# Kernel optimization log

Measured on AMD Instinct MI355X. Metric: run time of the kernel, lower is better.

The kernel has to match this reference:

```python
import jax, jax.numpy as jnp
import numpy as np

B, S, D, H = 2, 2048, 1024, 16
HW = D // H  # head width = 64


def setup_inputs() -> dict:
    key = jax.random.key(0)
    ks = jax.random.split(key, 9)
    x = jax.random.normal(ks[0], (B, S, D), dtype=jnp.float32)
    mask = jax.random.randint(ks[1], (B, S), 0, 2, dtype=jnp.int32)
    pos = jax.random.normal(ks[2], (B, S, S), dtype=jnp.float32) * 0.02
    wq = jax.random.normal(ks[3], (D, D), dtype=jnp.float32) * 0.02
    bq = jnp.zeros((D,), dtype=jnp.float32)
    wk = jax.random.normal(ks[4], (D, D), dtype=jnp.float32) * 0.02
    bk = jnp.zeros((D,), dtype=jnp.float32)
    wv = jax.random.normal(ks[5], (D, D), dtype=jnp.float32) * 0.02
    bv = jnp.zeros((D,), dtype=jnp.float32)
    return {"x": x, "mask": mask, "pos": pos,
            "wq": wq, "bq": bq, "wk": wk, "bk": bk, "wv": wv, "bv": bv}


def reference(x, mask, pos, wq, bq, wk, bk, wv, bv):
    # QKV projections (torch Linear: y = x @ W^T + b)
    q = (x @ wq.T + bq).reshape(B, S, H, HW)
    k = (x @ wk.T + bk).reshape(B, S, H, HW)
    v = (x @ wv.T + bv).reshape(B, S, H, HW)
    # scores: (B, H, Sq, Sk)
    scores = jnp.einsum('bqhd,bkhd->bhqk', q, k) / jnp.sqrt(jnp.float32(HW))
    scores = scores + pos[:, None, :, :]
    m = mask.astype(jnp.float32)[:, None, None, :]
    scores = scores - 10000.0 * (1.0 - m)
    attn = jax.nn.softmax(scores, axis=-1)  # dropout p=0 (inference)
    h = jnp.einsum('bhqk,bkhd->bqhd', attn, v).reshape(B, S, D)
    return h
```

## Files before the change

### kernel.cpp

```cpp
#include <hip/hip_runtime.h>

#define B_ 2
#define S_ 2048
#define D_ 1024
#define H_ 16
#define HW_ 64
#define NT_ (S_ / 64)

typedef __attribute__((ext_vector_type(8))) short s16x8;
typedef __attribute__((ext_vector_type(4))) float f32x4;
typedef __attribute__((ext_vector_type(2))) unsigned int u32x2;
typedef __attribute__((ext_vector_type(4))) unsigned int u32x4;

__device__ __forceinline__ unsigned short f2bf(float f) {
  unsigned int x = __builtin_bit_cast(unsigned int, f);
  x += 0x7fffu + ((x >> 16) & 1u);
  return (unsigned short)(x >> 16);
}
__device__ __forceinline__ unsigned int cvtpk_bf16(float lo, float hi) {
  unsigned int r;
  asm("v_cvt_pk_bf16_f32 %0, %1, %2" : "=v"(r) : "v"(lo), "v"(hi));
  return r;
}
__device__ __forceinline__ void gload16(const void* g, void* l) {
  __builtin_amdgcn_global_load_lds(
      (const __attribute__((address_space(1))) unsigned int*)g,
      (__attribute__((address_space(3))) unsigned int*)l, 16, 0, 0);
}

__global__ __launch_bounds__(256) void cvt_f32_bf16(const float* __restrict__ src,
                                                    unsigned short* __restrict__ dst,
                                                    int n8) {
  int i = blockIdx.x * 256 + threadIdx.x;
  if (i >= n8) return;
  const float4* s = (const float4*)src;
  float4 a = s[2 * i], b = s[2 * i + 1];
  s16x8 o;
  o[0] = (short)f2bf(a.x); o[1] = (short)f2bf(a.y);
  o[2] = (short)f2bf(a.z); o[3] = (short)f2bf(a.w);
  o[4] = (short)f2bf(b.x); o[5] = (short)f2bf(b.y);
  o[6] = (short)f2bf(b.z); o[7] = (short)f2bf(b.w);
  ((s16x8*)dst)[i] = o;
}

__global__ __launch_bounds__(256) void cvt_w3(const float* __restrict__ wq,
                                              const float* __restrict__ wk,
                                              const float* __restrict__ wv,
                                              unsigned short* __restrict__ dst) {
  int blk = blockIdx.x;
  const float* src = (blk < 512) ? wq : (blk < 1024) ? wk : wv;
  int i = (blk & 511) * 256 + threadIdx.x;
  const float4* s = (const float4*)src;
  float4 a = s[2 * i], b = s[2 * i + 1];
  s16x8 o;
  o[0] = (short)f2bf(a.x); o[1] = (short)f2bf(a.y);
  o[2] = (short)f2bf(a.z); o[3] = (short)f2bf(a.w);
  o[4] = (short)f2bf(b.x); o[5] = (short)f2bf(b.y);
  o[6] = (short)f2bf(b.z); o[7] = (short)f2bf(b.w);
  ((s16x8*)dst)[(size_t)(blk >> 9) * (D_ * D_ / 8) + i] = o;
}

__global__ __launch_bounds__(256) void cvt_pos(const float* __restrict__ pos,
                                               const int* __restrict__ mask,
                                               unsigned short* __restrict__ dst) {
  int i = blockIdx.x * 256 + threadIdx.x;
  int e = i * 8;
  int b = e / (S_ * S_);
  int k = e & (S_ - 1);
  const float4* s = (const float4*)pos;
  float4 a = s[2 * i], c = s[2 * i + 1];
  const int* mrow = mask + b * S_ + k;
  const float L2E = 1.4426950408889634f;
  float f[8] = {a.x, a.y, a.z, a.w, c.x, c.y, c.z, c.w};
  s16x8 o;
#pragma unroll
  for (int j = 0; j < 8; ++j) {
    float bias = mrow[j] ? 0.0f : -14427.0f;
    o[j] = (short)f2bf(f[j] * L2E + bias);
  }
  ((s16x8*)dst)[i] = o;
}

__global__ __launch_bounds__(256) void qkv_gemm(const unsigned short* __restrict__ X,
                                                const unsigned short* __restrict__ W3,
                                                const float* __restrict__ bq,
                                                const float* __restrict__ bk,
                                                const float* __restrict__ bv,
                                                unsigned short* __restrict__ O3) {
  const int mat = blockIdx.z;
  const unsigned short* Wp = W3 + (size_t)mat * (D_ * D_);
  const float* bias = (mat == 0) ? bq : (mat == 1) ? bk : bv;
  unsigned short* Op = O3 + (size_t)mat * ((size_t)B_ * S_ * D_);

  const int bm = blockIdx.y * 128, bn = blockIdx.x * 128;
  const int tid = threadIdx.x;
  const int lane = tid & 63, w = tid >> 6;
  const int wr = (w >> 1) * 64, wc = (w & 1) * 64;
  const int l15 = lane & 15, lh = lane >> 4;

  __shared__ __align__(16) unsigned short Al[128 * 64];
  __shared__ __align__(16) unsigned short Wl[128 * 64];

  f32x4 acc[4][4];
#pragma unroll
  for (int m = 0; m < 4; ++m)
#pragma unroll
    for (int n = 0; n < 4; ++n) acc[m][n] = (f32x4){0.f, 0.f, 0.f, 0.f};

  const int srow = lane >> 3;
  const int scol = ((lane & 7) ^ srow) * 8;
  const int i0 = w * 4;

  for (int k0 = 0; k0 < D_; k0 += 64) {
    __syncthreads();
#pragma unroll
    for (int i2 = 0; i2 < 4; ++i2) {
      int i = i0 + i2;
      int row = 8 * i + srow;
      gload16(X + (size_t)(bm + row) * D_ + k0 + scol, Al + i * 512);
      gload16(Wp + (size_t)(bn + row) * D_ + k0 + scol, Wl + i * 512);
    }
    __syncthreads();
#pragma unroll
    for (int kb = 0; kb < 2; ++kb) {
      const int cs = (kb * 32 + lh * 8) ^ ((l15 & 7) * 8);
      s16x8 af[4], wf[4];
#pragma unroll
      for (int m = 0; m < 4; ++m)
        af[m] = *(const s16x8*)(Al + (wr + m * 16 + l15) * 64 + cs);
#pragma unroll
      for (int n = 0; n < 4; ++n)
        wf[n] = *(const s16x8*)(Wl + (wc + n * 16 + l15) * 64 + cs);
#pragma unroll
      for (int m = 0; m < 4; ++m)
#pragma unroll
        for (int n = 0; n < 4; ++n)
          acc[m][n] =
              __builtin_amdgcn_mfma_f32_16x16x32_bf16(af[m], wf[n], acc[m][n], 0, 0, 0);
    }
  }

  const float oscale = (mat == 0) ? 0.18033688751411092f : 1.0f;
#pragma unroll
  for (int n = 0; n < 4; ++n) {
    int col = bn + wc + n * 16 + l15;
    float bval = bias[col];
#pragma unroll
    for (int m = 0; m < 4; ++m) {
      int row0 = bm + wr + m * 16 + lh * 4;
#pragma unroll
      for (int r = 0; r < 4; ++r)
        Op[(size_t)(row0 + r) * D_ + col] = f2bf((acc[m][n][r] + bval) * oscale);
    }
  }
}

__global__ __launch_bounds__(256) void vt_kernel(const unsigned short* __restrict__ Vin,
                                                 unsigned short* __restrict__ VT) {
  __shared__ unsigned short t[64][65];
  const int st = blockIdx.x, h = blockIdx.y, b = blockIdx.z;
  const int tid = threadIdx.x;
  const int r = tid >> 3, s = tid & 7;
#pragma unroll
  for (int i = 0; i < 2; ++i) {
    int key = i * 32 + r;
    s16x8 v = *(const s16x8*)(Vin + (size_t)(b * S_ + st * 64 + key) * D_ + h * HW_ + s * 8);
#pragma unroll
    for (int j = 0; j < 8; ++j) t[key][s * 8 + j] = (unsigned short)v[j];
  }
  __syncthreads();
#pragma unroll
  for (int i = 0; i < 2; ++i) {
    int d = i * 32 + r;
    s16x8 v;
#pragma unroll
    for (int j = 0; j < 8; ++j) v[j] = (short)t[s * 8 + j][d];
    *(s16x8*)(VT + ((size_t)(b * H_ + h) * HW_ + d) * S_ + st * 64 + s * 8) = v;
  }
}

__global__ __launch_bounds__(256, 4) void attn_kernel(
    const unsigned short* __restrict__ Q,
    const unsigned short* __restrict__ K,
    const unsigned short* __restrict__ VT,
    const unsigned short* __restrict__ POSM,
    float* __restrict__ OUT) {
  const int h = blockIdx.x, qt = blockIdx.y, b = blockIdx.z;
  const int tid = threadIdx.x;
  const int lane = tid & 63, w = tid >> 6;
  const int l15 = lane & 15, lh = lane >> 4;

  __shared__ __align__(16) unsigned short Kl[2][64 * 64];
  __shared__ __align__(16) unsigned short Vl[2][64 * 64];

  const int swzk = ((l15 & 3) | (((l15 >> 2) & 1) << 2)) * 8;
  const int swzv = ((l15 & 3) | ((l15 & 8) >> 1)) * 8;
  const int rowbase = 8 * (l15 >> 2) + (l15 & 3);

  const int srow = lane >> 3;
  const int scol = ((lane & 7) ^ ((lane >> 3) & 3) ^ ((w & 1) << 2)) * 8;
  const unsigned short* Kbase = K + (size_t)b * S_ * D_ + h * HW_;
  const unsigned short* Vbase = VT + ((size_t)(b * H_ + h) * HW_) * S_;

  auto stage = [&](int buf, int kt) {
    const int k0 = kt * 64;
#pragma unroll
    for (int i = 0; i < 2; ++i) {
      const int rb = i * 32 + w * 8;
      gload16(Kbase + (size_t)(k0 + rb + srow) * D_ + scol, &Kl[buf][rb * 64]);
      gload16(Vbase + (size_t)(rb + srow) * S_ + k0 + scol, &Vl[buf][rb * 64]);
    }
  };

  stage(0, 0);

  const int q0 = qt * 64 + w * 16;
  const int qg = q0 + l15;
  s16x8 qf[2];
  {
    const unsigned short* qp = Q + (size_t)(b * S_ + qg) * D_ + h * HW_ + lh * 8;
    qf[0] = *(const s16x8*)qp;
    qf[1] = *(const s16x8*)(qp + 32);
  }

  f32x4 Oc[4];
#pragma unroll
  for (int n = 0; n < 4; ++n) Oc[n] = (f32x4){0.f, 0.f, 0.f, 0.f};
  float mrow = -1e30f, lrow = 0.f;

  const unsigned short* Pp = POSM + (size_t)(b * S_ + qg) * S_ + lh * 8;

  for (int kt = 0; kt < NT_; ++kt) {
    const int cur = kt & 1;

    u32x2 pmw[4];
#pragma unroll
    for (int n = 0; n < 4; ++n)
      pmw[n] = *(const u32x2*)(Pp + kt * 64 + (n >> 1) * 32 + (n & 1) * 4);

    if (kt + 1 < NT_) {
      stage(cur ^ 1, kt + 1);
      asm volatile("s_waitcnt vmcnt(8)" ::: "memory");
    } else {
      asm volatile("s_waitcnt vmcnt(4)" ::: "memory");
    }
    asm volatile("s_barrier" ::: "memory");

    const unsigned short* Kc = Kl[cur];
    const unsigned short* Vc = Vl[cur];

    f32x4 sc[4];
    __builtin_amdgcn_s_setprio(1);
#pragma unroll
    for (int n = 0; n < 4; ++n) {
      const unsigned short* kr = Kc + (rowbase + (n & 1) * 4 + (n >> 1) * 32) * 64;
      s16x8 kf0 = *(const s16x8*)(kr + ((lh * 8) ^ swzk));
      s16x8 kf1 = *(const s16x8*)(kr + ((32 + lh * 8) ^ swzk));
      f32x4 c;
      c[0] = __builtin_bit_cast(float, pmw[n][0] << 16);
      c[1] = __builtin_bit_cast(float, pmw[n][0] & 0xffff0000u);
      c[2] = __builtin_bit_cast(float, pmw[n][1] << 16);
      c[3] = __builtin_bit_cast(float, pmw[n][1] & 0xffff0000u);
      c = __builtin_amdgcn_mfma_f32_16x16x32_bf16(kf0, qf[0], c, 0, 0, 0);
      c = __builtin_amdgcn_mfma_f32_16x16x32_bf16(kf1, qf[1], c, 0, 0, 0);
      sc[n] = c;
    }
    __builtin_amdgcn_s_setprio(0);

    float v0 = fmaxf(fmaxf(sc[0][0], sc[0][1]), fmaxf(sc[0][2], sc[0][3]));
    float v1 = fmaxf(fmaxf(sc[1][0], sc[1][1]), fmaxf(sc[1][2], sc[1][3]));
    float v2 = fmaxf(fmaxf(sc[2][0], sc[2][1]), fmaxf(sc[2][2], sc[2][3]));
    float v3 = fmaxf(fmaxf(sc[3][0], sc[3][1]), fmaxf(sc[3][2], sc[3][3]));
    float pmax = fmaxf(fmaxf(v0, v1), fmaxf(v2, v3));
    pmax = fmaxf(pmax, __shfl_xor(pmax, 16, 64));
    pmax = fmaxf(pmax, __shfl_xor(pmax, 32, 64));

    if (!__all(pmax - mrow <= 8.0f)) {
      float mnew = fmaxf(mrow, pmax);
      float alpha = exp2f(mrow - mnew);
      lrow *= alpha;
#pragma unroll
      for (int n = 0; n < 4; ++n)
#pragma unroll
        for (int r = 0; r < 4; ++r) Oc[n][r] *= alpha;
      mrow = mnew;
    }

    float rsum = 0.f;
#pragma unroll
    for (int n = 0; n < 4; ++n)
#pragma unroll
      for (int r = 0; r < 4; ++r) {
        float p = exp2f(sc[n][r] - mrow);
        sc[n][r] = p;
        rsum += p;
      }
    rsum += __shfl_xor(rsum, 16, 64);
    rsum += __shfl_xor(rsum, 32, 64);
    lrow += rsum;

    __builtin_amdgcn_s_setprio(1);
#pragma unroll
    for (int kb = 0; kb < 2; ++kb) {
      u32x4 pw;
      pw[0] = cvtpk_bf16(sc[2 * kb][0], sc[2 * kb][1]);
      pw[1] = cvtpk_bf16(sc[2 * kb][2], sc[2 * kb][3]);
      pw[2] = cvtpk_bf16(sc[2 * kb + 1][0], sc[2 * kb + 1][1]);
      pw[3] = cvtpk_bf16(sc[2 * kb + 1][2], sc[2 * kb + 1][3]);
      s16x8 pf = __builtin_bit_cast(s16x8, pw);
#pragma unroll
      for (int n = 0; n < 4; ++n) {
        s16x8 vf = *(const s16x8*)(Vc + (n * 16 + l15) * 64 + ((kb * 32 + lh * 8) ^ swzv));
        Oc[n] = __builtin_amdgcn_mfma_f32_16x16x32_bf16(vf, pf, Oc[n], 0, 0, 0);
      }
    }
    __builtin_amdgcn_s_setprio(0);

    asm volatile("s_barrier" ::: "memory");
  }

  float inv = 1.0f / lrow;
  float* outp = OUT + (size_t)(b * S_ + qg) * D_ + h * HW_ + lh * 4;
#pragma unroll
  for (int n = 0; n < 4; ++n) {
    f32x4 o;
#pragma unroll
    for (int r = 0; r < 4; ++r) o[r] = Oc[n][r] * inv;
    *(f32x4*)(outp + n * 16) = o;
  }
}

extern "C" void kernel_launch(void* const* d_in, const int* in_sizes, int n_in,
                              void* d_out, int out_size, void* d_ws, size_t ws_size,
                              hipStream_t stream) {
  const float* x   = (const float*)d_in[0];
  const int*   msk = (const int*)d_in[1];
  const float* pos = (const float*)d_in[2];
  const float* wq  = (const float*)d_in[3];
  const float* bq  = (const float*)d_in[4];
  const float* wk  = (const float*)d_in[5];
  const float* bk  = (const float*)d_in[6];
  const float* wv  = (const float*)d_in[7];
  const float* bv  = (const float*)d_in[8];
  float* out = (float*)d_out;

  char* ws = (char*)d_ws;
  unsigned short* xb   = (unsigned short*)(ws);
  unsigned short* wb   = (unsigned short*)(ws + 8388608);
  unsigned short* qkv  = (unsigned short*)(ws + 14680064);
  unsigned short* posb = (unsigned short*)(ws + 39845888);
  unsigned short* vt   = (unsigned short*)(ws + 56623104);

  cvt_f32_bf16<<<2048, 256, 0, stream>>>(x, xb, (B_ * S_ * D_) / 8);
  cvt_w3<<<1536, 256, 0, stream>>>(wq, wk, wv, wb);
  cvt_pos<<<4096, 256, 0, stream>>>(pos, msk, posb);

  qkv_gemm<<<dim3(D_ / 128, (B_ * S_) / 128, 3), 256, 0, stream>>>(
      xb, wb, bq, bk, bv, qkv);

  vt_kernel<<<dim3(S_ / 64, H_, B_), 256, 0, stream>>>(
      qkv + 2 * (size_t)B_ * S_ * D_, vt);

  attn_kernel<<<dim3(H_, S_ / 64, B_), 256, 0, stream>>>(
      qkv, qkv + (size_t)B_ * S_ * D_, vt, posb, out);
}
```

Measured before the change: 147.5 us.

## Merge conversion kernels, fuse V transpose into GEMM, prefetch pos bias

The three fp32-to-bf16 conversion kernels become one launch. The V transpose kernel is removed: the GEMM swaps MFMA operands for the V matrix and writes the transposed layout directly from its epilogue. The attention kernel now loads the next tile's position/mask bias one iteration ahead, with wait counts adjusted to match, and computes the row max with three-input max calls. This cuts launch overhead and one full pass over V, at the cost of scattered 2-byte stores in the V epilogue and extra registers for the prefetch.

```diff
diff --git a/kernel.cpp b/kernel.cpp
--- a/kernel.cpp
+++ b/kernel.cpp
@@ -22,63 +22,65 @@
   asm("v_cvt_pk_bf16_f32 %0, %1, %2" : "=v"(r) : "v"(lo), "v"(hi));
   return r;
 }
+__device__ __forceinline__ float max3f(float a, float b, float c) {
+  return fmaxf(fmaxf(a, b), c);
+}
 __device__ __forceinline__ void gload16(const void* g, void* l) {
   __builtin_amdgcn_global_load_lds(
       (const __attribute__((address_space(1))) unsigned int*)g,
       (__attribute__((address_space(3))) unsigned int*)l, 16, 0, 0);
 }
 
-__global__ __launch_bounds__(256) void cvt_f32_bf16(const float* __restrict__ src,
-                                                    unsigned short* __restrict__ dst,
-                                                    int n8) {
-  int i = blockIdx.x * 256 + threadIdx.x;
-  if (i >= n8) return;
-  const float4* s = (const float4*)src;
-  float4 a = s[2 * i], b = s[2 * i + 1];
-  s16x8 o;
-  o[0] = (short)f2bf(a.x); o[1] = (short)f2bf(a.y);
-  o[2] = (short)f2bf(a.z); o[3] = (short)f2bf(a.w);
-  o[4] = (short)f2bf(b.x); o[5] = (short)f2bf(b.y);
-  o[6] = (short)f2bf(b.z); o[7] = (short)f2bf(b.w);
-  ((s16x8*)dst)[i] = o;
-}
-
-__global__ __launch_bounds__(256) void cvt_w3(const float* __restrict__ wq,
-                                              const float* __restrict__ wk,
-                                              const float* __restrict__ wv,
-                                              unsigned short* __restrict__ dst) {
-  int blk = blockIdx.x;
-  const float* src = (blk < 512) ? wq : (blk < 1024) ? wk : wv;
-  int i = (blk & 511) * 256 + threadIdx.x;
-  const float4* s = (const float4*)src;
-  float4 a = s[2 * i], b = s[2 * i + 1];
-  s16x8 o;
-  o[0] = (short)f2bf(a.x); o[1] = (short)f2bf(a.y);
-  o[2] = (short)f2bf(a.z); o[3] = (short)f2bf(a.w);
-  o[4] = (short)f2bf(b.x); o[5] = (short)f2bf(b.y);
-  o[6] = (short)f2bf(b.z); o[7] = (short)f2bf(b.w);
-  ((s16x8*)dst)[(size_t)(blk >> 9) * (D_ * D_ / 8) + i] = o;
-}
-
-__global__ __launch_bounds__(256) void cvt_pos(const float* __restrict__ pos,
+__global__ __launch_bounds__(256) void cvt_all(const float* __restrict__ x,
+                                               const float* __restrict__ wq,
+                                               const float* __restrict__ wk,
+                                               const float* __restrict__ wv,
+                                               const float* __restrict__ pos,
                                                const int* __restrict__ mask,
-                                               unsigned short* __restrict__ dst) {
-  int i = blockIdx.x * 256 + threadIdx.x;
-  int e = i * 8;
-  int b = e / (S_ * S_);
-  int k = e & (S_ - 1);
-  const float4* s = (const float4*)pos;
-  float4 a = s[2 * i], c = s[2 * i + 1];
-  const int* mrow = mask + b * S_ + k;
-  const float L2E = 1.4426950408889634f;
-  float f[8] = {a.x, a.y, a.z, a.w, c.x, c.y, c.z, c.w};
-  s16x8 o;
-#pragma unroll
-  for (int j = 0; j < 8; ++j) {
-    float bias = mrow[j] ? 0.0f : -14427.0f;
-    o[j] = (short)f2bf(f[j] * L2E + bias);
-  }
-  ((s16x8*)dst)[i] = o;
+                                               unsigned short* __restrict__ xb,
+                                               unsigned short* __restrict__ wb,
+                                               unsigned short* __restrict__ posb) {
+  const int blk = blockIdx.x;
+  if (blk < 2048) {
+    int i = blk * 256 + threadIdx.x;
+    const float4* s = (const float4*)x;
+    float4 a = s[2 * i], b = s[2 * i + 1];
+    s16x8 o;
+    o[0] = (short)f2bf(a.x); o[1] = (short)f2bf(a.y);
+    o[2] = (short)f2bf(a.z); o[3] = (short)f2bf(a.w);
+    o[4] = (short)f2bf(b.x); o[5] = (short)f2bf(b.y);
+    o[6] = (short)f2bf(b.z); o[7] = (short)f2bf(b.w);
+    ((s16x8*)xb)[i] = o;
+  } else if (blk < 3584) {
+    int blk2 = blk - 2048;
+    const float* src = (blk2 < 512) ? wq : (blk2 < 1024) ? wk : wv;
+    int i = (blk2 & 511) * 256 + threadIdx.x;
+    const float4* s = (const float4*)src;
+    float4 a = s[2 * i], b = s[2 * i + 1];
+    s16x8 o;
+    o[0] = (short)f2bf(a.x); o[1] = (short)f2bf(a.y);
+    o[2] = (short)f2bf(a.z); o[3] = (short)f2bf(a.w);
+    o[4] = (short)f2bf(b.x); o[5] = (short)f2bf(b.y);
+    o[6] = (short)f2bf(b.z); o[7] = (short)f2bf(b.w);
+    ((s16x8*)wb)[(size_t)(blk2 >> 9) * (D_ * D_ / 8) + i] = o;
+  } else {
+    int i = (blk - 3584) * 256 + threadIdx.x;
+    int e = i * 8;
+    int b = e / (S_ * S_);
+    int k = e & (S_ - 1);
+    const float4* s = (const float4*)pos;
+    float4 a = s[2 * i], c = s[2 * i + 1];
+    const int* mrow = mask + b * S_ + k;
+    const float L2E = 1.4426950408889634f;
+    float f[8] = {a.x, a.y, a.z, a.w, c.x, c.y, c.z, c.w};
+    s16x8 o;
+#pragma unroll
+    for (int j = 0; j < 8; ++j) {
+      float bias = mrow[j] ? 0.0f : -14427.0f;
+      o[j] = (short)f2bf(f[j] * L2E + bias);
+    }
+    ((s16x8*)posb)[i] = o;
+  }
 }
 
 __global__ __launch_bounds__(256) void qkv_gemm(const unsigned short* __restrict__ X,
@@ -86,7 +88,8 @@
                                                 const float* __restrict__ bq,
                                                 const float* __restrict__ bk,
                                                 const float* __restrict__ bv,
-                                                unsigned short* __restrict__ O3) {
+                                                unsigned short* __restrict__ O3,
+                                                unsigned short* __restrict__ VT) {
   const int mat = blockIdx.z;
   const unsigned short* Wp = W3 + (size_t)mat * (D_ * D_);
   const float* bias = (mat == 0) ? bq : (mat == 1) ? bk : bv;
@@ -131,51 +134,54 @@
 #pragma unroll
       for (int n = 0; n < 4; ++n)
         wf[n] = *(const s16x8*)(Wl + (wc + n * 16 + l15) * 64 + cs);
-#pragma unroll
-      for (int m = 0; m < 4; ++m)
-#pragma unroll
-        for (int n = 0; n < 4; ++n)
-          acc[m][n] =
-              __builtin_amdgcn_mfma_f32_16x16x32_bf16(af[m], wf[n], acc[m][n], 0, 0, 0);
-    }
-  }
-
-  const float oscale = (mat == 0) ? 0.18033688751411092f : 1.0f;
-#pragma unroll
-  for (int n = 0; n < 4; ++n) {
-    int col = bn + wc + n * 16 + l15;
-    float bval = bias[col];
-#pragma unroll
-    for (int m = 0; m < 4; ++m) {
-      int row0 = bm + wr + m * 16 + lh * 4;
-#pragma unroll
-      for (int r = 0; r < 4; ++r)
-        Op[(size_t)(row0 + r) * D_ + col] = f2bf((acc[m][n][r] + bval) * oscale);
-    }
-  }
-}
-
-__global__ __launch_bounds__(256) void vt_kernel(const unsigned short* __restrict__ Vin,
-                                                 unsigned short* __restrict__ VT) {
-  __shared__ unsigned short t[64][65];
-  const int st = blockIdx.x, h = blockIdx.y, b = blockIdx.z;
-  const int tid = threadIdx.x;
-  const int r = tid >> 3, s = tid & 7;
-#pragma unroll
-  for (int i = 0; i < 2; ++i) {
-    int key = i * 32 + r;
-    s16x8 v = *(const s16x8*)(Vin + (size_t)(b * S_ + st * 64 + key) * D_ + h * HW_ + s * 8);
-#pragma unroll
-    for (int j = 0; j < 8; ++j) t[key][s * 8 + j] = (unsigned short)v[j];
-  }
-  __syncthreads();
-#pragma unroll
-  for (int i = 0; i < 2; ++i) {
-    int d = i * 32 + r;
-    s16x8 v;
-#pragma unroll
-    for (int j = 0; j < 8; ++j) v[j] = (short)t[s * 8 + j][d];
-    *(s16x8*)(VT + ((size_t)(b * H_ + h) * HW_ + d) * S_ + st * 64 + s * 8) = v;
+      if (mat == 2) {
+#pragma unroll
+        for (int m = 0; m < 4; ++m)
+#pragma unroll
+          for (int n = 0; n < 4; ++n)
+            acc[m][n] =
+                __builtin_amdgcn_mfma_f32_16x16x32_bf16(wf[n], af[m], acc[m][n], 0, 0, 0);
+      } else {
+#pragma unroll
+        for (int m = 0; m < 4; ++m)
+#pragma unroll
+          for (int n = 0; n < 4; ++n)
+            acc[m][n] =
+                __builtin_amdgcn_mfma_f32_16x16x32_bf16(af[m], wf[n], acc[m][n], 0, 0, 0);
+      }
+    }
+  }
+
+  if (mat == 2) {
+#pragma unroll
+    for (int n = 0; n < 4; ++n) {
+      f32x4 b4 = *(const f32x4*)(bias + bn + wc + n * 16 + lh * 4);
+#pragma unroll
+      for (int m = 0; m < 4; ++m) {
+        int t = bm + wr + m * 16 + l15;
+        int bb = t >> 11, s = t & (S_ - 1);
+#pragma unroll
+        for (int r = 0; r < 4; ++r) {
+          int f = bn + wc + n * 16 + lh * 4 + r;
+          VT[((size_t)(bb * H_ + (f >> 6)) * HW_ + (f & 63)) * S_ + s] =
+              f2bf(acc[m][n][r] + b4[r]);
+        }
+      }
+    }
+  } else {
+    const float oscale = (mat == 0) ? 0.18033688751411092f : 1.0f;
+#pragma unroll
+    for (int n = 0; n < 4; ++n) {
+      int col = bn + wc + n * 16 + l15;
+      float bval = bias[col];
+#pragma unroll
+      for (int m = 0; m < 4; ++m) {
+        int row0 = bm + wr + m * 16 + lh * 4;
+#pragma unroll
+        for (int r = 0; r < 4; ++r)
+          Op[(size_t)(row0 + r) * D_ + col] = f2bf((acc[m][n][r] + bval) * oscale);
+      }
+    }
   }
 }
 
@@ -212,10 +218,16 @@
     }
   };
 
-  stage(0, 0);
-
   const int q0 = qt * 64 + w * 16;
   const int qg = q0 + l15;
+  const unsigned short* Pp = POSM + (size_t)(b * S_ + qg) * S_ + lh * 8;
+
+  u32x2 pmw_c[4], pmw_n[4];
+#pragma unroll
+  for (int n = 0; n < 4; ++n)
+    pmw_c[n] = *(const u32x2*)(Pp + (n >> 1) * 32 + (n & 1) * 4);
+  stage(0, 0);
+
   s16x8 qf[2];
   {
     const unsigned short* qp = Q + (size_t)(b * S_ + qg) * D_ + h * HW_ + lh * 8;
@@ -228,21 +240,17 @@
   for (int n = 0; n < 4; ++n) Oc[n] = (f32x4){0.f, 0.f, 0.f, 0.f};
   float mrow = -1e30f, lrow = 0.f;
 
-  const unsigned short* Pp = POSM + (size_t)(b * S_ + qg) * S_ + lh * 8;
-
   for (int kt = 0; kt < NT_; ++kt) {
     const int cur = kt & 1;
 
-    u32x2 pmw[4];
-#pragma unroll
-    for (int n = 0; n < 4; ++n)
-      pmw[n] = *(const u32x2*)(Pp + kt * 64 + (n >> 1) * 32 + (n & 1) * 4);
-
     if (kt + 1 < NT_) {
+#pragma unroll
+      for (int n = 0; n < 4; ++n)
+        pmw_n[n] = *(const u32x2*)(Pp + (kt + 1) * 64 + (n >> 1) * 32 + (n & 1) * 4);
       stage(cur ^ 1, kt + 1);
-      asm volatile("s_waitcnt vmcnt(8)" ::: "memory");
+      asm volatile("s_waitcnt vmcnt(12)" ::: "memory");
     } else {
-      asm volatile("s_waitcnt vmcnt(4)" ::: "memory");
+      asm volatile("s_waitcnt vmcnt(0)" ::: "memory");
     }
     asm volatile("s_barrier" ::: "memory");
 
@@ -257,21 +265,24 @@
       s16x8 kf0 = *(const s16x8*)(kr + ((lh * 8) ^ swzk));
       s16x8 kf1 = *(const s16x8*)(kr + ((32 + lh * 8) ^ swzk));
       f32x4 c;
-      c[0] = __builtin_bit_cast(float, pmw[n][0] << 16);
-      c[1] = __builtin_bit_cast(float, pmw[n][0] & 0xffff0000u);
-      c[2] = __builtin_bit_cast(float, pmw[n][1] << 16);
-      c[3] = __builtin_bit_cast(float, pmw[n][1] & 0xffff0000u);
+      c[0] = __builtin_bit_cast(float, pmw_c[n][0] << 16);
+      c[1] = __builtin_bit_cast(float, pmw_c[n][0] & 0xffff0000u);
+      c[2] = __builtin_bit_cast(float, pmw_c[n][1] << 16);
+      c[3] = __builtin_bit_cast(float, pmw_c[n][1] & 0xffff0000u);
       c = __builtin_amdgcn_mfma_f32_16x16x32_bf16(kf0, qf[0], c, 0, 0, 0);
       c = __builtin_amdgcn_mfma_f32_16x16x32_bf16(kf1, qf[1], c, 0, 0, 0);
       sc[n] = c;
     }
     __builtin_amdgcn_s_setprio(0);
 
-    float v0 = fmaxf(fmaxf(sc[0][0], sc[0][1]), fmaxf(sc[0][2], sc[0][3]));
-    float v1 = fmaxf(fmaxf(sc[1][0], sc[1][1]), fmaxf(sc[1][2], sc[1][3]));
-    float v2 = fmaxf(fmaxf(sc[2][0], sc[2][1]), fmaxf(sc[2][2], sc[2][3]));
-    float v3 = fmaxf(fmaxf(sc[3][0], sc[3][1]), fmaxf(sc[3][2], sc[3][3]));
-    float pmax = fmaxf(fmaxf(v0, v1), fmaxf(v2, v3));
+    float pmax = max3f(sc[0][0], sc[0][1], sc[0][2]);
+    pmax = max3f(pmax, sc[0][3], sc[1][0]);
+    pmax = max3f(pmax, sc[1][1], sc[1][2]);
+    pmax = max3f(pmax, sc[1][3], sc[2][0]);
+    pmax = max3f(pmax, sc[2][1], sc[2][2]);
+    pmax = max3f(pmax, sc[2][3], sc[3][0]);
+    pmax = max3f(pmax, sc[3][1], sc[3][2]);
+    pmax = fmaxf(pmax, sc[3][3]);
     pmax = fmaxf(pmax, __shfl_xor(pmax, 16, 64));
     pmax = fmaxf(pmax, __shfl_xor(pmax, 32, 64));
 
@@ -317,6 +328,9 @@
     __builtin_amdgcn_s_setprio(0);
 
     asm volatile("s_barrier" ::: "memory");
+
+#pragma unroll
+    for (int n = 0; n < 4; ++n) pmw_c[n] = pmw_n[n];
   }
 
   float inv = 1.0f / lrow;
@@ -351,15 +365,10 @@
   unsigned short* posb = (unsigned short*)(ws + 39845888);
   unsigned short* vt   = (unsigned short*)(ws + 56623104);
 
-  cvt_f32_bf16<<<2048, 256, 0, stream>>>(x, xb, (B_ * S_ * D_) / 8);
-  cvt_w3<<<1536, 256, 0, stream>>>(wq, wk, wv, wb);
-  cvt_pos<<<4096, 256, 0, stream>>>(pos, msk, posb);
+  cvt_all<<<7680, 256, 0, stream>>>(x, wq, wk, wv, pos, msk, xb, wb, posb);
 
   qkv_gemm<<<dim3(D_ / 128, (B_ * S_) / 128, 3), 256, 0, stream>>>(
-      xb, wb, bq, bk, bv, qkv);
-
-  vt_kernel<<<dim3(S_ / 64, H_, B_), 256, 0, stream>>>(
-      qkv + 2 * (size_t)B_ * S_ * D_, vt);
+      xb, wb, bq, bk, bv, qkv, vt);
 
   attn_kernel<<<dim3(H_, S_ / 64, B_), 256, 0, stream>>>(
       qkv, qkv + (size_t)B_ * S_ * D_, vt, posb, out);
```

Result: faster. 136.2 us (-7.7%).
